# Optimization experiments

Measured on AMD Instinct MI355X. Metric: run time of the kernel, lower is better.

The kernel has to match this reference:

```python
import jax, jax.numpy as jnp
import numpy as np

B, N, H, L, V = 512, 20, 450, 56, 780
T = 2 * (N - 1)  # DFS trace length per tree (down+up edge per non-root node)


def _build(rng):
    EpT = 2 * (N - 1)
    n_nodes, n_edges = B * N, B * EpT
    src = np.zeros(n_edges, np.int32); dst = np.zeros(n_edges, np.int32)
    step_eid = np.zeros((T, B), np.int32)
    step_v = np.zeros((T, B), np.int32)
    p_flag = np.zeros((T, B), np.int32)
    for b in range(B):
        par = [0] * N
        ch = [[] for _ in range(N)]
        for i in range(1, N):
            p = int(rng.integers(max(0, i - 3), i))
            par[i] = p; ch[p].append(i)
        eo, no = b * EpT, b * N
        for i in range(1, N):
            d, u = eo + 2 * (i - 1), eo + 2 * (i - 1) + 1
            src[d], dst[d] = no + par[i], no + i
            src[u], dst[u] = no + i, no + par[i]
        trace = []
        stack = [(0, iter(ch[0]))]
        while stack:
            u_, it = stack[-1]
            c = next(it, None)
            if c is None:
                stack.pop()
                if stack:
                    pu = stack[-1][0]
                    trace.append((eo + 2 * (u_ - 1) + 1, no + pu, 0))
            else:
                trace.append((eo + 2 * (c - 1), no + c, 1))
                stack.append((c, iter(ch[c])))
        for t, (e, v, p) in enumerate(trace):
            step_eid[t, b], step_v[t, b], p_flag[t, b] = e, v, p
    return src, dst, step_eid, step_v, p_flag


def setup_inputs() -> dict:
    rng = np.random.default_rng(0)
    src, dst, step_eid, step_v, p_flag = _build(rng)
    n_nodes, n_edges = B * N, B * 2 * (N - 1)
    in_lists = [[] for _ in range(n_nodes)]
    for e in range(n_edges):
        in_lists[dst[e]].append(e)
    Dn = max(len(l) for l in in_lists)
    node_in = np.full((n_nodes, Dn), n_edges, np.int32)  # pad with sentinel n_edges
    for v, l in enumerate(in_lists):
        node_in[v, :len(l)] = l
    # line-graph (non-backtracking) predecessors of edge e=(u,v): edges (w,u), w != v
    preds = [[e2 for e2 in in_lists[src[e]] if src[e2] != dst[e]] for e in range(n_edges)]
    P = max(1, max(len(l) for l in preds))
    edge_pred = np.full((n_edges, P), n_edges, np.int32)
    for e, l in enumerate(preds):
        edge_pred[e, :len(l)] = l
    wid = rng.integers(0, V, n_nodes).astype(np.int32)
    root_ids = (np.arange(B) * N).astype(np.int32)
    # q rows: root block, then per-step rows where node is new (down edges)
    q_rows = list(range(B)); q_tgt = [int(wid[r]) for r in root_ids]
    for t in range(T):
        for b in range(B):
            if p_flag[t, b]:
                q_rows.append((t + 1) * B + b)
                q_tgt.append(int(wid[step_v[t, b]]))
    p_tgt = np.concatenate([p_flag.reshape(-1), np.zeros(B, np.int32)]).astype(np.int32)
    key = jax.random.key(0)
    def W(k, *shape):
        return jax.random.normal(jax.random.fold_in(key, k), shape, jnp.float32) * 0.05
    return dict(
        tree_vec=W(0, B, L), emb=W(1, V, H),
        Wz=W(2, 2 * H, H), bz=jnp.zeros(H, jnp.float32),
        Wh=W(3, 2 * H, H), bh=jnp.zeros(H, jnp.float32),
        Wr=W(4, H, H), Ur=W(5, H, H), br=jnp.zeros(H, jnp.float32),
        Ww=W(6, H + L, H), bw=jnp.zeros(H, jnp.float32),
        Uw=W(7, 2 * H + L, H), bu=jnp.zeros(H, jnp.float32),
        Wo=W(8, H, V), bo=jnp.zeros(V, jnp.float32),
        Us=W(9, H, 1), bs=jnp.zeros(1, jnp.float32),
        wid=jnp.asarray(wid), root_ids=jnp.asarray(root_ids),
        edge_src=jnp.asarray(src), edge_dst=jnp.asarray(dst),
        edge_pred=jnp.asarray(edge_pred), node_in=jnp.asarray(node_in),
        step_eid=jnp.asarray(step_eid), step_v=jnp.asarray(step_v),
        q_rows=jnp.asarray(np.array(q_rows, np.int32)),
        q_tgt=jnp.asarray(np.array(q_tgt, np.int32)),
        p_tgt=jnp.asarray(p_tgt),
    )


def reference(tree_vec, emb, Wz, bz, Wh, bh, Wr, Ur, br, Ww, bw, Uw, bu, Wo, bo, Us, bs,
              wid, root_ids, edge_src, edge_dst, edge_pred, node_in, step_eid, step_v,
              q_rows, q_tgt, p_tgt):
    n_edges = edge_src.shape[0]
    x = emb[wid]                              # [n_nodes, H] node embeddings
    src_x = x[edge_src]; dst_x = x[edge_dst]  # [n_edges, H]
    m0 = jnp.zeros((n_edges + 1, H), x.dtype)  # +1 sentinel zero row for padding

    def step(carry, inp):
        m, rm = carry
        eid, v = inp                          # [B] edge ids / dst node ids this DFS step
        pred = edge_pred[eid]                 # [B, P] non-backtracking predecessor edges
        s = m[pred].sum(1)                    # sum of incoming m
        arm = rm[pred].sum(1)                 # sum of incoming r*m
        sx = src_x[eid]; dx = dst_x[eid]
        z = jax.nn.sigmoid(jnp.concatenate([sx, s], 1) @ Wz + bz)
        m_new = (1 - z) * s + z * jnp.tanh(jnp.concatenate([sx, arm], 1) @ Wh + bh)
        r = jax.nn.sigmoid(dx @ Wr + m_new @ Ur + br)
        m = m.at[eid].set(m_new)
        rm = rm.at[eid].set(r * m_new)
        h = m[node_in[v]].sum(1)              # node pull: h_v = sum of incoming m
        return (m, rm), h

    _, h_steps = jax.lax.scan(step, (m0, m0), (step_eid, step_v))  # [T, B, H]

    x_root = x[root_ids]
    h_root = jnp.zeros_like(x_root)           # roots pulled before any edge update
    x_steps = x[step_v]                        # [T, B, H]
    tv_steps = jnp.broadcast_to(tree_vec[None], (T, B, L))
    p_root = jnp.concatenate([x_root, h_root, tree_vec], 1)[None]
    p_step = jnp.concatenate([x_steps, h_steps, tv_steps], 2)
    p_in = jnp.concatenate([p_root, p_step], 0).reshape((T + 1) * B, 2 * H + L)
    q_root = jnp.concatenate([h_root, tree_vec], 1)[None]
    q_step = jnp.concatenate([h_steps, tv_steps], 2)
    q_in = jnp.concatenate([q_root, q_step], 0).reshape((T + 1) * B, H + L)[q_rows]

    q_logits = jax.nn.relu(q_in @ Ww + bw) @ Wo + bo          # [nq, V]
    p_logit = (jax.nn.relu(p_in @ Uw + bu) @ Us + bs)[:, 0]   # [np]
    tgt = p_tgt.astype(p_logit.dtype)
    p_loss = jnp.sum(jnp.logaddexp(0.0, p_logit) - p_logit * tgt) / B
    lse = jax.nn.logsumexp(q_logits, axis=1)
    q_loss = jnp.sum(lse - jnp.take_along_axis(q_logits, q_tgt[:, None], 1)[:, 0]) / B
    p_acc = jnp.mean(((p_logit > 0).astype(p_tgt.dtype) == p_tgt).astype(jnp.float32))
    q_acc = jnp.mean((jnp.argmax(q_logits, 1).astype(q_tgt.dtype) == q_tgt).astype(jnp.float32))
    return (q_loss, p_loss, q_acc, p_acc)
```

## Files before the change

kernel.cpp:

```cpp
#include <hip/hip_runtime.h>
#include <math.h>

#define B_ 512
#define N_ 20
#define H_ 450
#define L_ 56
#define V_ 780
#define T_ 38
#define NNODES (B_*N_)
#define NEDGES (B_*2*(N_-1))
#define NPROWS ((T_+1)*B_)
#define KS 480
#define NT 4
#define AST 488
#define HSTR 456
#define KQ 512
#define KPP 992
#define LDL 784

typedef __attribute__((ext_vector_type(8))) short bf16x8;
typedef __attribute__((ext_vector_type(4))) float f32x4;

__device__ __forceinline__ float sigmoidf_(float v){ return 1.0f/(1.0f+expf(-v)); }

__device__ __forceinline__ unsigned short f2b(float x){
  unsigned int u = __float_as_uint(x);
  unsigned int r = (u + 0x7fffu + ((u >> 16) & 1u)) >> 16;
  return (unsigned short)r;
}
__device__ __forceinline__ float b2f(unsigned int v){
  return __uint_as_float((v & 0xffffu) << 16);
}
__device__ __forceinline__ unsigned int pack2(float lo, float hi){
  return (unsigned int)f2b(lo) | ((unsigned int)f2b(hi) << 16);
}

__global__ __launch_bounds__(256) void k_gather_xb(const float* __restrict__ emb,
    const int* __restrict__ wid, unsigned short* __restrict__ xb){
  int w = blockIdx.x*4 + (threadIdx.x>>6), lane = threadIdx.x & 63;
  if (w >= NNODES) return;
  const float2* src = (const float2*)(emb + (size_t)wid[w]*H_);
  unsigned int* dst = (unsigned int*)(xb + (size_t)w*KS);
  for (int j2 = lane; j2 < 240; j2 += 64){
    unsigned int v = 0;
    if (j2 < 225){ float2 f = src[j2]; v = pack2(f.x, f.y); }
    dst[j2] = v;
  }
}

__global__ void k_wtall(const float* __restrict__ Wz, const float* __restrict__ Wh,
    const float* __restrict__ Ur, const float* __restrict__ Wr,
    const float* __restrict__ Ww, const float* __restrict__ Uw,
    const float* __restrict__ Wo, const float* __restrict__ tv,
    unsigned short* __restrict__ WzB, unsigned short* __restrict__ WhB,
    unsigned short* __restrict__ UrT, unsigned short* __restrict__ WzTop,
    unsigned short* __restrict__ WhTop, unsigned short* __restrict__ WrT,
    unsigned short* __restrict__ WwT, unsigned short* __restrict__ UwT,
    unsigned short* __restrict__ WoT, unsigned short* __restrict__ tvb){
  int bid = blockIdx.x;
  if (bid < 512*6){
    int seg = bid >> 9, c = bid & 511;
    const float* src; unsigned short* dst; int rowbase;
    switch(seg){
      case 0: src = Wz; dst = WzB; rowbase = 450; break;
      case 1: src = Wh; dst = WhB; rowbase = 450; break;
      case 2: src = Ur; dst = UrT; rowbase = 0; break;
      case 3: src = Wz; dst = WzTop; rowbase = 0; break;
      case 4: src = Wh; dst = WhTop; rowbase = 0; break;
      default: src = Wr; dst = WrT; rowbase = 0; break;
    }
    unsigned short* drow = dst + (size_t)c*KS;
    for (int k = threadIdx.x; k < KS; k += blockDim.x){
      float v = 0.f;
      if (c < 450 && k < 450) v = src[(size_t)(rowbase + k)*450 + c];
      drow[k] = f2b(v);
    }
  } else if (bid < 512*7){
    int c = bid - 512*6;
    unsigned short* drow = WwT + (size_t)c*KQ;
    for (int k = threadIdx.x; k < KQ; k += blockDim.x){
      float v = 0.f;
      if (c < 450){
        if (k < 450) v = Ww[(size_t)k*450 + c];
        else if (k >= 456) v = Ww[(size_t)(450 + k - 456)*450 + c];
      }
      drow[k] = f2b(v);
    }
  } else if (bid < 512*8){
    int c = bid - 512*7;
    unsigned short* drow = UwT + (size_t)c*KPP;
    for (int k = threadIdx.x; k < KPP; k += blockDim.x){
      float v = 0.f;
      if (c < 450){
        if (k < 450) v = Uw[(size_t)k*450 + c];
        else if (k >= 480 && k < 930) v = Uw[(size_t)(450 + k - 480)*450 + c];
        else if (k >= 936) v = Uw[(size_t)(900 + k - 936)*450 + c];
      }
      drow[k] = f2b(v);
    }
  } else if (bid < 512*8 + 832){
    int c = bid - 512*8;
    unsigned short* drow = WoT + (size_t)c*512;
    for (int k = threadIdx.x; k < 512; k += blockDim.x){
      float v = 0.f;
      if (c < V_ && k < 450) v = Wo[(size_t)k*V_ + c];
      drow[k] = f2b(v);
    }
  } else {
    int b = bid - (512*8 + 832);
    unsigned short* drow = tvb + (size_t)b*64;
    for (int k = threadIdx.x; k < 64; k += blockDim.x)
      drow[k] = f2b((k < L_) ? tv[b*L_ + k] : 0.f);
  }
}

struct ScanP {
  const unsigned short *WzB, *WhB, *UrT;
  const unsigned short *XWz, *XWh, *XWr;
  const int *edge_src, *edge_dst, *step_eid;
  unsigned short *m, *rm;
  unsigned short *hm, *hrm;
  unsigned short *hb;
};

__global__ __launch_bounds__(1024, 4) void k_scan_tree(ScanP p){
  __shared__ unsigned short A1s[16*AST];
  __shared__ unsigned short A2s[16*AST];
  __shared__ unsigned short A3s[16*AST];
  __shared__ unsigned short sZ[NT*HSTR], sH[NT*HSTR], sR[NT*HSTR];
  __shared__ int s_eoff[T_][NT], s_roff[T_][NT], s_srcH[T_][NT], s_dstH[T_][NT];

  const int tid = threadIdx.x;
  const int lane = tid & 63, l15 = lane & 15, kh = lane >> 4, ko = kh*8;
  const int wv = tid >> 6;
  const int r0 = blockIdx.x * NT;
  const int c_0 = wv*32 + l15, c_1 = c_0 + 16;

  const unsigned short* pWz0 = p.WzB + (size_t)c_0*KS;
  const unsigned short* pWz1 = p.WzB + (size_t)c_1*KS;
  const unsigned short* pWh0 = p.WhB + (size_t)c_0*KS;
  const unsigned short* pWh1 = p.WhB + (size_t)c_1*KS;
  const unsigned short* pUr0 = p.UrT + (size_t)c_0*KS;
  const unsigned short* pUr1 = p.UrT + (size_t)c_1*KS;
  const unsigned short* aA1 = A1s + l15*AST;
  const unsigned short* aA2 = A2s + l15*AST;
  const unsigned short* aA3 = A3s + l15*AST;

  for (int idx = tid; idx < 16*AST; idx += 1024){ A1s[idx] = 0; A2s[idx] = 0; A3s[idx] = 0; }
  for (int idx = tid; idx < T_*NT; idx += 1024){
    int t = idx >> 2, rl = idx & 3;
    int e = p.step_eid[t*B_ + r0 + rl];
    s_eoff[t][rl] = e*KS;
    s_roff[t][rl] = (e ^ 1)*KS;
    s_srcH[t][rl] = p.edge_src[e]*HSTR;
    s_dstH[t][rl] = p.edge_dst[e]*HSTR;
  }
  __syncthreads();

  for (int t = 0; t < T_; ++t){
    bf16x8 bz0[3], bz1[3], bh0[3], bh1[3];
    #pragma unroll
    for (int i = 0; i < 3; ++i){
      bz0[i] = *(const bf16x8*)(pWz0 + i*32 + ko);
      bz1[i] = *(const bf16x8*)(pWz1 + i*32 + ko);
      bh0[i] = *(const bf16x8*)(pWh0 + i*32 + ko);
      bh1[i] = *(const bf16x8*)(pWh1 + i*32 + ko);
    }

    if (tid < 228){
      int rl = tid / 57, g = tid - rl*57;
      int j = g*8;
      uint4 hm4 = *(const uint4*)(p.hm  + s_srcH[t][rl] + j);
      uint4 hr4 = *(const uint4*)(p.hrm + s_srcH[t][rl] + j);
      uint4 mr4 = *(const uint4*)(p.m   + s_roff[t][rl] + j);
      uint4 rr4 = *(const uint4*)(p.rm  + s_roff[t][rl] + j);
      uint4 o1, o2;
      o1.x = pack2(b2f(hm4.x)-b2f(mr4.x), b2f(hm4.x>>16)-b2f(mr4.x>>16));
      o1.y = pack2(b2f(hm4.y)-b2f(mr4.y), b2f(hm4.y>>16)-b2f(mr4.y>>16));
      o1.z = pack2(b2f(hm4.z)-b2f(mr4.z), b2f(hm4.z>>16)-b2f(mr4.z>>16));
      o1.w = pack2(b2f(hm4.w)-b2f(mr4.w), b2f(hm4.w>>16)-b2f(mr4.w>>16));
      o2.x = pack2(b2f(hr4.x)-b2f(rr4.x), b2f(hr4.x>>16)-b2f(rr4.x>>16));
      o2.y = pack2(b2f(hr4.y)-b2f(rr4.y), b2f(hr4.y>>16)-b2f(rr4.y>>16));
      o2.z = pack2(b2f(hr4.z)-b2f(rr4.z), b2f(hr4.z>>16)-b2f(rr4.z>>16));
      o2.w = pack2(b2f(hr4.w)-b2f(rr4.w), b2f(hr4.w>>16)-b2f(rr4.w>>16));
      *(uint4*)(A1s + rl*AST + j) = o1;
      *(uint4*)(A2s + rl*AST + j) = o2;
    } else if (tid < 912){
      int idx2 = tid - 228;
      int mat = idx2 / 228, rem = idx2 - mat*228;
      int rl = rem / 57, g = rem - rl*57;
      int row = (mat == 2) ? s_dstH[t][rl] : s_srcH[t][rl];
      const unsigned short* src = (mat == 0) ? p.XWz : (mat == 1) ? p.XWh : p.XWr;
      unsigned short* d = (mat == 0) ? sZ : (mat == 1) ? sH : sR;
      *(uint4*)(d + rl*HSTR + g*8) = *(const uint4*)(src + row + g*8);
    }
    __syncthreads();

    f32x4 accZ0 = {}, accZ1 = {}, accH0 = {}, accH1 = {};
    #pragma unroll
    for (int it = 0; it < 15; ++it){
      const int sl = it % 3;
      bf16x8 a1 = *(const bf16x8*)(aA1 + it*32 + ko);
      bf16x8 a2 = *(const bf16x8*)(aA2 + it*32 + ko);
      accZ0 = __builtin_amdgcn_mfma_f32_16x16x32_bf16(a1, bz0[sl], accZ0, 0,0,0);
      accZ1 = __builtin_amdgcn_mfma_f32_16x16x32_bf16(a1, bz1[sl], accZ1, 0,0,0);
      accH0 = __builtin_amdgcn_mfma_f32_16x16x32_bf16(a2, bh0[sl], accH0, 0,0,0);
      accH1 = __builtin_amdgcn_mfma_f32_16x16x32_bf16(a2, bh1[sl], accH1, 0,0,0);
      if (it + 3 < 15){
        bz0[sl] = *(const bf16x8*)(pWz0 + (it+3)*32 + ko);
        bz1[sl] = *(const bf16x8*)(pWz1 + (it+3)*32 + ko);
        bh0[sl] = *(const bf16x8*)(pWh0 + (it+3)*32 + ko);
        bh1[sl] = *(const bf16x8*)(pWh1 + (it+3)*32 + ko);
      }
    }

    bf16x8 bu0[3], bu1[3];
    #pragma unroll
    for (int i = 0; i < 3; ++i){
      bu0[i] = *(const bf16x8*)(pUr0 + i*32 + ko);
      bu1[i] = *(const bf16x8*)(pUr1 + i*32 + ko);
    }

    if (kh == 0){
      #pragma unroll
      for (int n = 0; n < 2; ++n){
        int cc = wv*32 + n*16 + l15;
        if (cc < H_){
          f32x4 aZ = n ? accZ1 : accZ0;
          f32x4 aH = n ? accH1 : accH0;
          #pragma unroll
          for (int reg = 0; reg < 4; ++reg){
            int rl = reg;
            float z  = sigmoidf_(aZ[reg] + b2f(sZ[rl*HSTR + cc]));
            float th = tanhf   (aH[reg] + b2f(sH[rl*HSTR + cc]));
            float s_ = b2f(A1s[rl*AST + cc]);
            float mn = (1.f - z)*s_ + z*th;
            unsigned short mb = f2b(mn);
            p.m[s_eoff[t][rl] + cc] = mb;
            A3s[rl*AST + cc] = mb;
            float hv = b2f(p.hm[s_dstH[t][rl] + cc]) + mn;
            p.hm[s_dstH[t][rl] + cc] = f2b(hv);
            p.hb[(size_t)(t*B_ + r0 + rl)*HSTR + cc] = f2b(hv);
          }
        }
      }
    }
    __syncthreads();

    f32x4 accR0 = {}, accR1 = {};
    #pragma unroll
    for (int it = 0; it < 15; ++it){
      const int sl = it % 3;
      bf16x8 a = *(const bf16x8*)(aA3 + it*32 + ko);
      accR0 = __builtin_amdgcn_mfma_f32_16x16x32_bf16(a, bu0[sl], accR0, 0,0,0);
      accR1 = __builtin_amdgcn_mfma_f32_16x16x32_bf16(a, bu1[sl], accR1, 0,0,0);
      if (it + 3 < 15){
        bu0[sl] = *(const bf16x8*)(pUr0 + (it+3)*32 + ko);
        bu1[sl] = *(const bf16x8*)(pUr1 + (it+3)*32 + ko);
      }
    }

    if (kh == 0){
      #pragma unroll
      for (int n = 0; n < 2; ++n){
        int cc = wv*32 + n*16 + l15;
        if (cc < H_){
          f32x4 aR = n ? accR1 : accR0;
          #pragma unroll
          for (int reg = 0; reg < 4; ++reg){
            int rl = reg;
            float r_ = sigmoidf_(aR[reg] + b2f(sR[rl*HSTR + cc]));
            float mn = b2f(A3s[rl*AST + cc]);
            float rv = r_*mn;
            p.rm[s_eoff[t][rl] + cc] = f2b(rv);
            float hv = b2f(p.hrm[s_dstH[t][rl] + cc]) + rv;
            p.hrm[s_dstH[t][rl] + cc] = f2b(hv);
          }
        }
      }
    }
    __syncthreads();
  }
}

__global__ __launch_bounds__(256) void k_head_mfma(
    const unsigned short* __restrict__ A, const unsigned short* __restrict__ BT, int K,
    const float* __restrict__ bias, int Nact, int relu,
    float* __restrict__ outF, int ldF, unsigned short* __restrict__ outB, int ldB)
{
  __shared__ unsigned short As[64*40], Bs[64*40];
  const int tid = threadIdx.x;
  const int gr0 = blockIdx.y*64, gc0 = blockIdx.x*64;
  const int lane = tid & 63;
  const int w = tid >> 6, wr = w >> 1, wc = w & 1;
  const int l15 = lane & 15, kh = lane >> 4;
  const int sr = tid >> 2, sj = (tid & 3) * 8;
  f32x4 acc[2][2] = {};
  for (int kt = 0; kt < K; kt += 32){
    __syncthreads();
    *(float4*)&As[sr*40 + sj] = *(const float4*)&A[(size_t)(gr0+sr)*K + kt + sj];
    *(float4*)&Bs[sr*40 + sj] = *(const float4*)&BT[(size_t)(gc0+sr)*K + kt + sj];
    __syncthreads();
    bf16x8 a0 = *(const bf16x8*)&As[(wr*32      + l15)*40 + kh*8];
    bf16x8 a1 = *(const bf16x8*)&As[(wr*32 + 16 + l15)*40 + kh*8];
    bf16x8 b0 = *(const bf16x8*)&Bs[(wc*32      + l15)*40 + kh*8];
    bf16x8 b1 = *(const bf16x8*)&Bs[(wc*32 + 16 + l15)*40 + kh*8];
    acc[0][0] = __builtin_amdgcn_mfma_f32_16x16x32_bf16(a0,b0,acc[0][0],0,0,0);
    acc[0][1] = __builtin_amdgcn_mfma_f32_16x16x32_bf16(a0,b1,acc[0][1],0,0,0);
    acc[1][0] = __builtin_amdgcn_mfma_f32_16x16x32_bf16(a1,b0,acc[1][0],0,0,0);
    acc[1][1] = __builtin_amdgcn_mfma_f32_16x16x32_bf16(a1,b1,acc[1][1],0,0,0);
  }
  #pragma unroll
  for (int mi = 0; mi < 2; ++mi){
    #pragma unroll
    for (int n = 0; n < 2; ++n){
      int c = gc0 + wc*32 + n*16 + l15;
      float bc = (c < Nact) ? bias[c] : 0.f;
      #pragma unroll
      for (int reg = 0; reg < 4; ++reg){
        int r = gr0 + wr*32 + mi*16 + kh*4 + reg;
        float v = acc[mi][n][reg] + bc;
        if (relu) v = fmaxf(v, 0.f);
        if (outF && c < Nact) outF[(size_t)r*ldF + c] = v;
        if (outB && c < ldB)  outB[(size_t)r*ldB + c] = (c < Nact) ? f2b(v) : (unsigned short)0;
      }
    }
  }
}

__global__ __launch_bounds__(256) void k_xw(const unsigned short* __restrict__ xb,
    const unsigned short* __restrict__ WzTop, const unsigned short* __restrict__ WhTop,
    const unsigned short* __restrict__ WrT,
    const float* __restrict__ bz, const float* __restrict__ bh, const float* __restrict__ br,
    unsigned short* __restrict__ XWz, unsigned short* __restrict__ XWh,
    unsigned short* __restrict__ XWr)
{
  __shared__ unsigned short As[64*40], Bs[64*40];
  const unsigned short* BT = (blockIdx.z == 0) ? WzTop : (blockIdx.z == 1) ? WhTop : WrT;
  const float* bias        = (blockIdx.z == 0) ? bz    : (blockIdx.z == 1) ? bh    : br;
  unsigned short* outB     = (blockIdx.z == 0) ? XWz   : (blockIdx.z == 1) ? XWh   : XWr;
  const int tid = threadIdx.x;
  const int gr0 = blockIdx.y*64, gc0 = blockIdx.x*64;
  const int lane = tid & 63;
  const int w = tid >> 6, wr = w >> 1, wc = w & 1;
  const int l15 = lane & 15, kh = lane >> 4;
  const int sr = tid >> 2, sj = (tid & 3) * 8;
  f32x4 acc[2][2] = {};
  for (int kt = 0; kt < KS; kt += 32){
    __syncthreads();
    *(float4*)&As[sr*40 + sj] = *(const float4*)&xb[(size_t)(gr0+sr)*KS + kt + sj];
    *(float4*)&Bs[sr*40 + sj] = *(const float4*)&BT[(size_t)(gc0+sr)*KS + kt + sj];
    __syncthreads();
    bf16x8 a0 = *(const bf16x8*)&As[(wr*32      + l15)*40 + kh*8];
    bf16x8 a1 = *(const bf16x8*)&As[(wr*32 + 16 + l15)*40 + kh*8];
    bf16x8 b0 = *(const bf16x8*)&Bs[(wc*32      + l15)*40 + kh*8];
    bf16x8 b1 = *(const bf16x8*)&Bs[(wc*32 + 16 + l15)*40 + kh*8];
    acc[0][0] = __builtin_amdgcn_mfma_f32_16x16x32_bf16(a0,b0,acc[0][0],0,0,0);
    acc[0][1] = __builtin_amdgcn_mfma_f32_16x16x32_bf16(a0,b1,acc[0][1],0,0,0);
    acc[1][0] = __builtin_amdgcn_mfma_f32_16x16x32_bf16(a1,b0,acc[1][0],0,0,0);
    acc[1][1] = __builtin_amdgcn_mfma_f32_16x16x32_bf16(a1,b1,acc[1][1],0,0,0);
  }
  #pragma unroll
  for (int mi = 0; mi < 2; ++mi){
    #pragma unroll
    for (int n = 0; n < 2; ++n){
      int c = gc0 + wc*32 + n*16 + l15;
      if (c >= HSTR) continue;
      float bc = (c < H_) ? bias[c] : 0.f;
      #pragma unroll
      for (int reg = 0; reg < 4; ++reg){
        int r = gr0 + wr*32 + mi*16 + kh*4 + reg;
        outB[(size_t)r*HSTR + c] = (c < H_) ? f2b(acc[mi][n][reg] + bc) : (unsigned short)0;
      }
    }
  }
}

__global__ __launch_bounds__(256) void k_head_q(const unsigned short* __restrict__ hb,
    const unsigned short* __restrict__ tvb, const int* __restrict__ q_rows,
    const unsigned short* __restrict__ BT, const float* __restrict__ bw,
    unsigned short* __restrict__ hqb, int nq)
{
  __shared__ unsigned short As[64*40], Bs[64*40];
  __shared__ int s_hrow[64], s_b[64];
  const int tid = threadIdx.x;
  const int gr0 = blockIdx.y*64, gc0 = blockIdx.x*64;
  if (tid < 64){
    int gi = gr0 + tid;
    int row = (gi < nq) ? q_rows[gi] : 0;
    s_hrow[tid] = (row < B_) ? -1 : row - B_;
    s_b[tid] = row & (B_-1);
  }
  const int lane = tid & 63;
  const int w = tid >> 6, wr = w >> 1, wc = w & 1;
  const int l15 = lane & 15, kh = lane >> 4;
  const int sr = tid >> 2, sj = (tid & 3) * 8;
  f32x4 acc[2][2] = {};
  for (int kt = 0; kt < KQ; kt += 32){
    __syncthreads();
    int gk = kt + sj;
    uint4 av;
    if (gk < 456){
      int hr = s_hrow[sr];
      if (hr < 0){ av.x = av.y = av.z = av.w = 0u; }
      else av = *(const uint4*)(hb + (size_t)hr*HSTR + gk);
    } else {
      av = *(const uint4*)(tvb + (size_t)s_b[sr]*64 + (gk - 456));
    }
    *(uint4*)&As[sr*40 + sj] = av;
    *(float4*)&Bs[sr*40 + sj] = *(const float4*)&BT[(size_t)(gc0+sr)*KQ + gk];
    __syncthreads();
    bf16x8 a0 = *(const bf16x8*)&As[(wr*32      + l15)*40 + kh*8];
    bf16x8 a1 = *(const bf16x8*)&As[(wr*32 + 16 + l15)*40 + kh*8];
    bf16x8 b0 = *(const bf16x8*)&Bs[(wc*32      + l15)*40 + kh*8];
    bf16x8 b1 = *(const bf16x8*)&Bs[(wc*32 + 16 + l15)*40 + kh*8];
    acc[0][0] = __builtin_amdgcn_mfma_f32_16x16x32_bf16(a0,b0,acc[0][0],0,0,0);
    acc[0][1] = __builtin_amdgcn_mfma_f32_16x16x32_bf16(a0,b1,acc[0][1],0,0,0);
    acc[1][0] = __builtin_amdgcn_mfma_f32_16x16x32_bf16(a1,b0,acc[1][0],0,0,0);
    acc[1][1] = __builtin_amdgcn_mfma_f32_16x16x32_bf16(a1,b1,acc[1][1],0,0,0);
  }
  #pragma unroll
  for (int mi = 0; mi < 2; ++mi){
    #pragma unroll
    for (int n = 0; n < 2; ++n){
      int c = gc0 + wc*32 + n*16 + l15;
      float bc = (c < H_) ? bw[c] : 0.f;
      #pragma unroll
      for (int reg = 0; reg < 4; ++reg){
        int r = gr0 + wr*32 + mi*16 + kh*4 + reg;
        float v = fmaxf(acc[mi][n][reg] + bc, 0.f);
        hqb[(size_t)r*KQ + c] = (c < H_) ? f2b(v) : (unsigned short)0;
      }
    }
  }
}

__global__ __launch_bounds__(256) void k_head_p2(const unsigned short* __restrict__ xb,
    const unsigned short* __restrict__ hb, const unsigned short* __restrict__ tvb,
    const int* __restrict__ root_ids, const int* __restrict__ step_v,
    const unsigned short* __restrict__ BT, const float* __restrict__ bu_,
    const float* __restrict__ Us, float* __restrict__ plog)
{
  __shared__ unsigned short As[64*40], Bs[64*40];
  __shared__ int s_xrow[64], s_hrow[64], s_b[64];
  const int tid = threadIdx.x;
  const int gr0 = blockIdx.y*64, gc0 = blockIdx.x*64;
  if (tid < 64){
    int i = gr0 + tid;
    int b = i & (B_-1);
    s_b[tid] = b;
    s_xrow[tid] = (i < B_) ? root_ids[b] : step_v[i - B_];
    s_hrow[tid] = (i < B_) ? -1 : i - B_;
  }
  const int lane = tid & 63;
  const int w = tid >> 6, wr = w >> 1, wc = w & 1;
  const int l15 = lane & 15, kh = lane >> 4;
  const int sr = tid >> 2, sj = (tid & 3) * 8;
  f32x4 acc[2][2] = {};
  for (int kt = 0; kt < KPP; kt += 32){
    __syncthreads();
    int gk = kt + sj;
    uint4 av;
    if (gk < 480){
      av = *(const uint4*)(xb + (size_t)s_xrow[sr]*KS + gk);
    } else if (gk < 936){
      int hr = s_hrow[sr];
      if (hr < 0){ av.x = av.y = av.z = av.w = 0u; }
      else av = *(const uint4*)(hb + (size_t)hr*HSTR + (gk - 480));
    } else {
      av = *(const uint4*)(tvb + (size_t)s_b[sr]*64 + (gk - 936));
    }
    *(uint4*)&As[sr*40 + sj] = av;
    *(float4*)&Bs[sr*40 + sj] = *(const float4*)&BT[(size_t)(gc0+sr)*KPP + gk];
    __syncthreads();
    bf16x8 a0 = *(const bf16x8*)&As[(wr*32      + l15)*40 + kh*8];
    bf16x8 a1 = *(const bf16x8*)&As[(wr*32 + 16 + l15)*40 + kh*8];
    bf16x8 b0 = *(const bf16x8*)&Bs[(wc*32      + l15)*40 + kh*8];
    bf16x8 b1 = *(const bf16x8*)&Bs[(wc*32 + 16 + l15)*40 + kh*8];
    acc[0][0] = __builtin_amdgcn_mfma_f32_16x16x32_bf16(a0,b0,acc[0][0],0,0,0);
    acc[0][1] = __builtin_amdgcn_mfma_f32_16x16x32_bf16(a0,b1,acc[0][1],0,0,0);
    acc[1][0] = __builtin_amdgcn_mfma_f32_16x16x32_bf16(a1,b0,acc[1][0],0,0,0);
    acc[1][1] = __builtin_amdgcn_mfma_f32_16x16x32_bf16(a1,b1,acc[1][1],0,0,0);
  }
  #pragma unroll
  for (int mi = 0; mi < 2; ++mi){
    float rowsum[4] = {0.f,0.f,0.f,0.f};
    #pragma unroll
    for (int n = 0; n < 2; ++n){
      int c = gc0 + wc*32 + n*16 + l15;
      float uc = 0.f, bc = 0.f;
      if (c < H_){ uc = Us[c]; bc = bu_[c]; }
      #pragma unroll
      for (int reg = 0; reg < 4; ++reg){
        float v = fmaxf(acc[mi][n][reg] + bc, 0.f);
        rowsum[reg] += (c < H_) ? v*uc : 0.f;
      }
    }
    #pragma unroll
    for (int reg = 0; reg < 4; ++reg){
      float pv = rowsum[reg];
      pv += __shfl_xor(pv,1); pv += __shfl_xor(pv,2);
      pv += __shfl_xor(pv,4); pv += __shfl_xor(pv,8);
      if (l15 == 0) atomicAdd(plog + gr0 + wr*32 + mi*16 + kh*4 + reg, pv);
    }
  }
}

__global__ __launch_bounds__(256) void k_qreduce3(const unsigned short* __restrict__ logits,
    const int* __restrict__ q_tgt, int nq, float* __restrict__ out){
  int w = blockIdx.x*4 + (threadIdx.x>>6), lane = threadIdx.x & 63;
  int nw = gridDim.x*4;
  float qloss = 0.f, qacc = 0.f;
  for (int i = w; i < nq; i += nw){
    const uint2* lr2 = (const uint2*)(logits + (size_t)i*LDL);
    uint2 vals[4]; int cnt = 0;
    float mx = -INFINITY; int mi = 0x7fffffff;
    for (int j4 = lane; j4 < 195; j4 += 64){
      uint2 v = lr2[j4]; vals[cnt++] = v;
      float e0 = b2f(v.x), e1 = b2f(v.x>>16), e2 = b2f(v.y), e3 = b2f(v.y>>16);
      if (e0 > mx){ mx = e0; mi = j4*4; }
      if (e1 > mx){ mx = e1; mi = j4*4+1; }
      if (e2 > mx){ mx = e2; mi = j4*4+2; }
      if (e3 > mx){ mx = e3; mi = j4*4+3; }
    }
    #pragma unroll
    for (int off = 32; off; off >>= 1){
      float omx = __shfl_xor(mx, off); int omi = __shfl_xor(mi, off);
      if (omx > mx || (omx == mx && omi < mi)){ mx = omx; mi = omi; }
    }
    float ps = 0.f; cnt = 0;
    for (int j4 = lane; j4 < 195; j4 += 64){
      uint2 v = vals[cnt++];
      ps += expf(b2f(v.x)-mx) + expf(b2f(v.x>>16)-mx)
          + expf(b2f(v.y)-mx) + expf(b2f(v.y>>16)-mx);
    }
    #pragma unroll
    for (int off = 32; off; off >>= 1) ps += __shfl_xor(ps, off);
    if (lane == 0){
      int tg = q_tgt[i];
      float lt = b2f((unsigned int)logits[(size_t)i*LDL + tg]);
      qloss += mx + logf(ps) - lt;
      qacc  += (mi == tg) ? 1.f : 0.f;
    }
  }
  if (lane == 0){
    atomicAdd(out+0, qloss*(1.0f/B_));
    atomicAdd(out+2, qacc *(1.0f/(float)nq));
  }
}

__global__ __launch_bounds__(256) void k_pfinal(const float* __restrict__ plog,
    const float* __restrict__ bs, const int* __restrict__ p_tgt, float* __restrict__ out){
  int i = blockIdx.x*256 + threadIdx.x;
  float loss = 0.f, acc = 0.f;
  if (i < NPROWS){
    float pl = plog[i] + bs[0];
    float tgt = (float)p_tgt[i];
    loss = fmaxf(pl, 0.f) + log1pf(expf(-fabsf(pl))) - pl*tgt;
    acc = (((pl > 0.f) ? 1 : 0) == p_tgt[i]) ? 1.f : 0.f;
  }
  #pragma unroll
  for (int off = 32; off; off >>= 1){
    loss += __shfl_xor(loss, off); acc += __shfl_xor(acc, off);
  }
  if ((threadIdx.x & 63) == 0){
    atomicAdd(out+1, loss*(1.0f/B_));
    atomicAdd(out+3, acc *(1.0f/(float)NPROWS));
  }
}

extern "C" void kernel_launch(void* const* d_in, const int* in_sizes, int n_in,
                              void* d_out, int out_size, void* d_ws, size_t ws_size,
                              hipStream_t stream){
  const float* tree_vec = (const float*)d_in[0];
  const float* emb  = (const float*)d_in[1];
  const float* Wz   = (const float*)d_in[2];
  const float* bz   = (const float*)d_in[3];
  const float* Wh   = (const float*)d_in[4];
  const float* bh   = (const float*)d_in[5];
  const float* Wr   = (const float*)d_in[6];
  const float* Ur   = (const float*)d_in[7];
  const float* br   = (const float*)d_in[8];
  const float* Ww   = (const float*)d_in[9];
  const float* bw   = (const float*)d_in[10];
  const float* Uw   = (const float*)d_in[11];
  const float* bu   = (const float*)d_in[12];
  const float* Wo   = (const float*)d_in[13];
  const float* bo   = (const float*)d_in[14];
  const float* Us   = (const float*)d_in[15];
  const float* bs   = (const float*)d_in[16];
  const int* wid      = (const int*)d_in[17];
  const int* root_ids = (const int*)d_in[18];
  const int* edge_src = (const int*)d_in[19];
  const int* edge_dst = (const int*)d_in[20];
  const int* step_eid = (const int*)d_in[23];
  const int* step_v   = (const int*)d_in[24];
  const int* q_rows   = (const int*)d_in[25];
  const int* q_tgt    = (const int*)d_in[26];
  const int* p_tgt    = (const int*)d_in[27];
  int nq = in_sizes[25];

  char* ws = (char*)d_ws;
  const size_t XB_OFF    = 0;
  const size_t HB_OFF    = 9830400;
  const size_t M_OFF     = 27574272;
  const size_t RM_OFF    = M_OFF + 18678784;
  const size_t HM_OFF    = RM_OFF + 18678784;
  const size_t HRM_OFF   = HM_OFF + 9338880;
  const size_t WZB_OFF   = HRM_OFF + 9338880;
  const size_t WHB_OFF   = WZB_OFF + 491520;
  const size_t URT_OFF   = WHB_OFF + 491520;
  const size_t WZTOP_OFF = URT_OFF + 491520;
  const size_t WHTOP_OFF = WZTOP_OFF + 491520;
  const size_t WRT_OFF   = WHTOP_OFF + 491520;
  const size_t WWT_OFF   = WRT_OFF + 491520;
  const size_t UWT_OFF   = WWT_OFF + 524288;
  const size_t WOT_OFF   = UWT_OFF + 1015808;
  const size_t TVB_OFF   = WOT_OFF + 851968;
  const size_t XWZ_OFF   = TVB_OFF + 65536;
  const size_t XWH_OFF   = XWZ_OFF + 9338880;
  const size_t XWR_OFF   = XWH_OFF + 9338880;
  const size_t LQ_OFF  = M_OFF;
  const size_t HQB_OFF = XWZ_OFF;
  const size_t PL_OFF  = XWH_OFF;

  unsigned short* xb = (unsigned short*)(ws + XB_OFF);
  unsigned short* hb = (unsigned short*)(ws + HB_OFF);
  unsigned short* m_ = (unsigned short*)(ws + M_OFF);
  unsigned short* rm = (unsigned short*)(ws + RM_OFF);
  unsigned short* hm = (unsigned short*)(ws + HM_OFF);
  unsigned short* hrm = (unsigned short*)(ws + HRM_OFF);
  unsigned short* WzB = (unsigned short*)(ws + WZB_OFF);
  unsigned short* WhB = (unsigned short*)(ws + WHB_OFF);
  unsigned short* UrT = (unsigned short*)(ws + URT_OFF);
  unsigned short* WzTop = (unsigned short*)(ws + WZTOP_OFF);
  unsigned short* WhTop = (unsigned short*)(ws + WHTOP_OFF);
  unsigned short* WrT = (unsigned short*)(ws + WRT_OFF);
  unsigned short* WwT = (unsigned short*)(ws + WWT_OFF);
  unsigned short* UwT = (unsigned short*)(ws + UWT_OFF);
  unsigned short* WoT = (unsigned short*)(ws + WOT_OFF);
  unsigned short* tvb = (unsigned short*)(ws + TVB_OFF);
  unsigned short* XWz = (unsigned short*)(ws + XWZ_OFF);
  unsigned short* XWh = (unsigned short*)(ws + XWH_OFF);
  unsigned short* XWr = (unsigned short*)(ws + XWR_OFF);

  hipMemsetAsync(ws + HB_OFF, 0, WZB_OFF - HB_OFF, stream);
  hipMemsetAsync(d_out, 0, (size_t)out_size*sizeof(float), stream);

  k_gather_xb<<<2560, 256, 0, stream>>>(emb, wid, xb);
  k_wtall<<<512*8 + 832 + 512, 256, 0, stream>>>(Wz, Wh, Ur, Wr, Ww, Uw, Wo, tree_vec,
      WzB, WhB, UrT, WzTop, WhTop, WrT, WwT, UwT, WoT, tvb);
  k_xw<<<dim3(8,160,3), 256, 0, stream>>>(xb, WzTop, WhTop, WrT, bz, bh, br, XWz, XWh, XWr);

  ScanP sp;
  sp.WzB = WzB; sp.WhB = WhB; sp.UrT = UrT;
  sp.XWz = XWz; sp.XWh = XWh; sp.XWr = XWr;
  sp.edge_src = edge_src; sp.edge_dst = edge_dst; sp.step_eid = step_eid;
  sp.m = m_; sp.rm = rm; sp.hm = hm; sp.hrm = hrm; sp.hb = hb;
  k_scan_tree<<<B_/NT, 1024, 0, stream>>>(sp);

  unsigned short* logitsq = (unsigned short*)(ws + LQ_OFF);
  unsigned short* hqb     = (unsigned short*)(ws + HQB_OFF);
  float* plog             = (float*)(ws + PL_OFF);
  hipMemsetAsync(plog, 0, (size_t)NPROWS*4, stream);

  k_head_q<<<dim3(8, nq/64), 256, 0, stream>>>(hb, tvb, q_rows, WwT, bw, hqb, nq);
  k_head_mfma<<<dim3(13, nq/64), 256, 0, stream>>>(hqb, WoT, 512, bo, V_, 0,
      nullptr, 0, logitsq, LDL);
  k_qreduce3<<<320, 256, 0, stream>>>(logitsq, q_tgt, nq, (float*)d_out);

  k_head_p2<<<dim3(8, NPROWS/64), 256, 0, stream>>>(xb, hb, tvb, root_ids, step_v,
      UwT, bu, Us, plog);
  k_pfinal<<<78, 256, 0, stream>>>(plog, bs, p_tgt, (float*)d_out);
}
```

Before: 1.322 ms.

## Keep per-tree message and node state in LDS, one tree per block

```diff
diff --git a/kernel.cpp b/kernel.cpp
--- a/kernel.cpp
+++ b/kernel.cpp
@@ -11,9 +11,8 @@
 #define NEDGES (B_*2*(N_-1))
 #define NPROWS ((T_+1)*B_)
 #define KS 480
-#define NT 4
-#define AST 488
 #define HSTR 456
+#define LST 456
 #define KQ 512
 #define KPP 992
 #define LDL 784
@@ -118,22 +117,22 @@
   const unsigned short *WzB, *WhB, *UrT;
   const unsigned short *XWz, *XWh, *XWr;
   const int *edge_src, *edge_dst, *step_eid;
-  unsigned short *m, *rm;
-  unsigned short *hm, *hrm;
   unsigned short *hb;
 };
 
 __global__ __launch_bounds__(1024, 4) void k_scan_tree(ScanP p){
-  __shared__ unsigned short A1s[16*AST];
-  __shared__ unsigned short A2s[16*AST];
-  __shared__ unsigned short A3s[16*AST];
-  __shared__ unsigned short sZ[NT*HSTR], sH[NT*HSTR], sR[NT*HSTR];
-  __shared__ int s_eoff[T_][NT], s_roff[T_][NT], s_srcH[T_][NT], s_dstH[T_][NT];
+  __shared__ unsigned short Lm[T_*LST];
+  __shared__ unsigned short Lrm[T_*LST];
+  __shared__ unsigned short Lhm[N_*LST];
+  __shared__ unsigned short Lhrm[N_*LST];
+  __shared__ unsigned short A1s[488], A2s[488], A3s[488];
+  __shared__ unsigned short sZ[456], sH[456], sR[456];
+  __shared__ int s_le[T_], s_lrev[T_], s_lsrc[T_], s_ldst[T_], s_gsrc[T_], s_gdst[T_];
 
   const int tid = threadIdx.x;
   const int lane = tid & 63, l15 = lane & 15, kh = lane >> 4, ko = kh*8;
   const int wv = tid >> 6;
-  const int r0 = blockIdx.x * NT;
+  const int b = blockIdx.x;
   const int c_0 = wv*32 + l15, c_1 = c_0 + 16;
 
   const unsigned short* pWz0 = p.WzB + (size_t)c_0*KS;
@@ -142,18 +141,20 @@
   const unsigned short* pWh1 = p.WhB + (size_t)c_1*KS;
   const unsigned short* pUr0 = p.UrT + (size_t)c_0*KS;
   const unsigned short* pUr1 = p.UrT + (size_t)c_1*KS;
-  const unsigned short* aA1 = A1s + l15*AST;
-  const unsigned short* aA2 = A2s + l15*AST;
-  const unsigned short* aA3 = A3s + l15*AST;
-
-  for (int idx = tid; idx < 16*AST; idx += 1024){ A1s[idx] = 0; A2s[idx] = 0; A3s[idx] = 0; }
-  for (int idx = tid; idx < T_*NT; idx += 1024){
-    int t = idx >> 2, rl = idx & 3;
-    int e = p.step_eid[t*B_ + r0 + rl];
-    s_eoff[t][rl] = e*KS;
-    s_roff[t][rl] = (e ^ 1)*KS;
-    s_srcH[t][rl] = p.edge_src[e]*HSTR;
-    s_dstH[t][rl] = p.edge_dst[e]*HSTR;
+
+  for (int i = tid; i < T_*LST; i += 1024){ Lm[i] = 0; Lrm[i] = 0; }
+  for (int i = tid; i < N_*LST; i += 1024){ Lhm[i] = 0; Lhrm[i] = 0; }
+  if (tid < 38){ A1s[450+tid] = 0; A2s[450+tid] = 0; A3s[450+tid] = 0; }
+  if (tid < T_){
+    int e = p.step_eid[tid*B_ + b];
+    int le = e - b*T_;
+    s_le[tid]   = le*LST;
+    s_lrev[tid] = (le ^ 1)*LST;
+    int sg = p.edge_src[e], dg = p.edge_dst[e];
+    s_lsrc[tid] = (sg - b*N_)*LST;
+    s_ldst[tid] = (dg - b*N_)*LST;
+    s_gsrc[tid] = sg*HSTR;
+    s_gdst[tid] = dg*HSTR;
   }
   __syncthreads();
 
@@ -167,32 +168,23 @@
       bh1[i] = *(const bf16x8*)(pWh1 + i*32 + ko);
     }
 
-    if (tid < 228){
-      int rl = tid / 57, g = tid - rl*57;
-      int j = g*8;
-      uint4 hm4 = *(const uint4*)(p.hm  + s_srcH[t][rl] + j);
-      uint4 hr4 = *(const uint4*)(p.hrm + s_srcH[t][rl] + j);
-      uint4 mr4 = *(const uint4*)(p.m   + s_roff[t][rl] + j);
-      uint4 rr4 = *(const uint4*)(p.rm  + s_roff[t][rl] + j);
-      uint4 o1, o2;
-      o1.x = pack2(b2f(hm4.x)-b2f(mr4.x), b2f(hm4.x>>16)-b2f(mr4.x>>16));
-      o1.y = pack2(b2f(hm4.y)-b2f(mr4.y), b2f(hm4.y>>16)-b2f(mr4.y>>16));
-      o1.z = pack2(b2f(hm4.z)-b2f(mr4.z), b2f(hm4.z>>16)-b2f(mr4.z>>16));
-      o1.w = pack2(b2f(hm4.w)-b2f(mr4.w), b2f(hm4.w>>16)-b2f(mr4.w>>16));
-      o2.x = pack2(b2f(hr4.x)-b2f(rr4.x), b2f(hr4.x>>16)-b2f(rr4.x>>16));
-      o2.y = pack2(b2f(hr4.y)-b2f(rr4.y), b2f(hr4.y>>16)-b2f(rr4.y>>16));
-      o2.z = pack2(b2f(hr4.z)-b2f(rr4.z), b2f(hr4.z>>16)-b2f(rr4.z>>16));
-      o2.w = pack2(b2f(hr4.w)-b2f(rr4.w), b2f(hr4.w>>16)-b2f(rr4.w>>16));
-      *(uint4*)(A1s + rl*AST + j) = o1;
-      *(uint4*)(A2s + rl*AST + j) = o2;
-    } else if (tid < 912){
-      int idx2 = tid - 228;
-      int mat = idx2 / 228, rem = idx2 - mat*228;
-      int rl = rem / 57, g = rem - rl*57;
-      int row = (mat == 2) ? s_dstH[t][rl] : s_srcH[t][rl];
+    if (tid < 225){
+      int j = tid*2;
+      unsigned int hm2 = *(const unsigned int*)(Lhm + s_lsrc[t] + j);
+      unsigned int m2  = *(const unsigned int*)(Lm  + s_lrev[t] + j);
+      *(unsigned int*)(A1s + j) = pack2(b2f(hm2)-b2f(m2), b2f(hm2>>16)-b2f(m2>>16));
+    } else if (tid >= 256 && tid < 481){
+      int j = (tid-256)*2;
+      unsigned int hr2 = *(const unsigned int*)(Lhrm + s_lsrc[t] + j);
+      unsigned int r2  = *(const unsigned int*)(Lrm  + s_lrev[t] + j);
+      *(unsigned int*)(A2s + j) = pack2(b2f(hr2)-b2f(r2), b2f(hr2>>16)-b2f(r2>>16));
+    } else if (tid >= 512 && tid < 683){
+      int idx = tid - 512;
+      int mat = idx / 57, g = idx - mat*57;
+      int row = (mat == 2) ? s_gdst[t] : s_gsrc[t];
       const unsigned short* src = (mat == 0) ? p.XWz : (mat == 1) ? p.XWh : p.XWr;
       unsigned short* d = (mat == 0) ? sZ : (mat == 1) ? sH : sR;
-      *(uint4*)(d + rl*HSTR + g*8) = *(const uint4*)(src + row + g*8);
+      *(uint4*)(d + g*8) = *(const uint4*)(src + row + g*8);
     }
     __syncthreads();
 
@@ -200,8 +192,8 @@
     #pragma unroll
     for (int it = 0; it < 15; ++it){
       const int sl = it % 3;
-      bf16x8 a1 = *(const bf16x8*)(aA1 + it*32 + ko);
-      bf16x8 a2 = *(const bf16x8*)(aA2 + it*32 + ko);
+      bf16x8 a1 = *(const bf16x8*)(A1s + it*32 + ko);
+      bf16x8 a2 = *(const bf16x8*)(A2s + it*32 + ko);
       accZ0 = __builtin_amdgcn_mfma_f32_16x16x32_bf16(a1, bz0[sl], accZ0, 0,0,0);
       accZ1 = __builtin_amdgcn_mfma_f32_16x16x32_bf16(a1, bz1[sl], accZ1, 0,0,0);
       accH0 = __builtin_amdgcn_mfma_f32_16x16x32_bf16(a2, bh0[sl], accH0, 0,0,0);
@@ -226,22 +218,18 @@
       for (int n = 0; n < 2; ++n){
         int cc = wv*32 + n*16 + l15;
         if (cc < H_){
-          f32x4 aZ = n ? accZ1 : accZ0;
-          f32x4 aH = n ? accH1 : accH0;
-          #pragma unroll
-          for (int reg = 0; reg < 4; ++reg){
-            int rl = reg;
-            float z  = sigmoidf_(aZ[reg] + b2f(sZ[rl*HSTR + cc]));
-            float th = tanhf   (aH[reg] + b2f(sH[rl*HSTR + cc]));
-            float s_ = b2f(A1s[rl*AST + cc]);
-            float mn = (1.f - z)*s_ + z*th;
-            unsigned short mb = f2b(mn);
-            p.m[s_eoff[t][rl] + cc] = mb;
-            A3s[rl*AST + cc] = mb;
-            float hv = b2f(p.hm[s_dstH[t][rl] + cc]) + mn;
-            p.hm[s_dstH[t][rl] + cc] = f2b(hv);
-            p.hb[(size_t)(t*B_ + r0 + rl)*HSTR + cc] = f2b(hv);
-          }
+          float aZ = n ? accZ1[0] : accZ0[0];
+          float aH = n ? accH1[0] : accH0[0];
+          float z  = sigmoidf_(aZ + b2f(sZ[cc]));
+          float th = tanhf   (aH + b2f(sH[cc]));
+          float s_ = b2f(A1s[cc]);
+          float mn = (1.f - z)*s_ + z*th;
+          unsigned short mb = f2b(mn);
+          Lm[s_le[t] + cc] = mb;
+          A3s[cc] = mb;
+          float hv = b2f(Lhm[s_ldst[t] + cc]) + mn;
+          Lhm[s_ldst[t] + cc] = f2b(hv);
+          p.hb[(size_t)(t*B_ + b)*HSTR + cc] = f2b(hv);
         }
       }
     }
@@ -251,7 +239,7 @@
     #pragma unroll
     for (int it = 0; it < 15; ++it){
       const int sl = it % 3;
-      bf16x8 a = *(const bf16x8*)(aA3 + it*32 + ko);
+      bf16x8 a = *(const bf16x8*)(A3s + it*32 + ko);
       accR0 = __builtin_amdgcn_mfma_f32_16x16x32_bf16(a, bu0[sl], accR0, 0,0,0);
       accR1 = __builtin_amdgcn_mfma_f32_16x16x32_bf16(a, bu1[sl], accR1, 0,0,0);
       if (it + 3 < 15){
@@ -265,17 +253,12 @@
       for (int n = 0; n < 2; ++n){
         int cc = wv*32 + n*16 + l15;
         if (cc < H_){
-          f32x4 aR = n ? accR1 : accR0;
-          #pragma unroll
-          for (int reg = 0; reg < 4; ++reg){
-            int rl = reg;
-            float r_ = sigmoidf_(aR[reg] + b2f(sR[rl*HSTR + cc]));
-            float mn = b2f(A3s[rl*AST + cc]);
-            float rv = r_*mn;
-            p.rm[s_eoff[t][rl] + cc] = f2b(rv);
-            float hv = b2f(p.hrm[s_dstH[t][rl] + cc]) + rv;
-            p.hrm[s_dstH[t][rl] + cc] = f2b(hv);
-          }
+          float aR = n ? accR1[0] : accR0[0];
+          float r_ = sigmoidf_(aR + b2f(sR[cc]));
+          float mn = b2f(A3s[cc]);
+          float rv = r_*mn;
+          Lrm[s_le[t] + cc] = f2b(rv);
+          Lhrm[s_ldst[t] + cc] = f2b(b2f(Lhrm[s_ldst[t] + cc]) + rv);
         }
       }
     }
@@ -603,11 +586,8 @@
   char* ws = (char*)d_ws;
   const size_t XB_OFF    = 0;
   const size_t HB_OFF    = 9830400;
-  const size_t M_OFF     = 27574272;
-  const size_t RM_OFF    = M_OFF + 18678784;
-  const size_t HM_OFF    = RM_OFF + 18678784;
-  const size_t HRM_OFF   = HM_OFF + 9338880;
-  const size_t WZB_OFF   = HRM_OFF + 9338880;
+  const size_t SCRATCH   = 27574272;
+  const size_t WZB_OFF   = 83609600;
   const size_t WHB_OFF   = WZB_OFF + 491520;
   const size_t URT_OFF   = WHB_OFF + 491520;
   const size_t WZTOP_OFF = URT_OFF + 491520;
@@ -620,16 +600,12 @@
   const size_t XWZ_OFF   = TVB_OFF + 65536;
   const size_t XWH_OFF   = XWZ_OFF + 9338880;
   const size_t XWR_OFF   = XWH_OFF + 9338880;
-  const size_t LQ_OFF  = M_OFF;
-  const size_t HQB_OFF = XWZ_OFF;
-  const size_t PL_OFF  = XWH_OFF;
+  const size_t LQ_OFF  = SCRATCH;
+  const size_t HQB_OFF = SCRATCH + 16056320;
+  const size_t PL_OFF  = HQB_OFF + 10485760;
 
   unsigned short* xb = (unsigned short*)(ws + XB_OFF);
   unsigned short* hb = (unsigned short*)(ws + HB_OFF);
-  unsigned short* m_ = (unsigned short*)(ws + M_OFF);
-  unsigned short* rm = (unsigned short*)(ws + RM_OFF);
-  unsigned short* hm = (unsigned short*)(ws + HM_OFF);
-  unsigned short* hrm = (unsigned short*)(ws + HRM_OFF);
   unsigned short* WzB = (unsigned short*)(ws + WZB_OFF);
   unsigned short* WhB = (unsigned short*)(ws + WHB_OFF);
   unsigned short* UrT = (unsigned short*)(ws + URT_OFF);
@@ -644,7 +620,7 @@
   unsigned short* XWh = (unsigned short*)(ws + XWH_OFF);
   unsigned short* XWr = (unsigned short*)(ws + XWR_OFF);
 
-  hipMemsetAsync(ws + HB_OFF, 0, WZB_OFF - HB_OFF, stream);
+  hipMemsetAsync(ws + HB_OFF, 0, 17743872ull, stream);
   hipMemsetAsync(d_out, 0, (size_t)out_size*sizeof(float), stream);
 
   k_gather_xb<<<2560, 256, 0, stream>>>(emb, wid, xb);
@@ -656,8 +632,8 @@
   sp.WzB = WzB; sp.WhB = WhB; sp.UrT = UrT;
   sp.XWz = XWz; sp.XWh = XWh; sp.XWr = XWr;
   sp.edge_src = edge_src; sp.edge_dst = edge_dst; sp.step_eid = step_eid;
-  sp.m = m_; sp.rm = rm; sp.hm = hm; sp.hrm = hrm; sp.hb = hb;
-  k_scan_tree<<<B_/NT, 1024, 0, stream>>>(sp);
+  sp.hb = hb;
+  k_scan_tree<<<B_, 1024, 0, stream>>>(sp);
 
   unsigned short* logitsq = (unsigned short*)(ws + LQ_OFF);
   unsigned short* hqb     = (unsigned short*)(ws + HQB_OFF);
```

Result: slower. 1.934 ms (+46.4%).
